# Performance work log

Hardware: AMD Instinct MI355X
Metric: run time of the kernel (lower is better)

Reference implementation:

```python
import jax, jax.numpy as jnp
import numpy as np

H = 128  # hidden_size


def lstm_layer(x, Wih, Whh, bih, bhh):
    """Unidirectional LSTM layer, batch_first input x: [B, T, I] -> [B, T, H].
    PyTorch gate order: i, f, g, o."""
    B = x.shape[0]
    # precompute input projections as one big GEMM: [B, T, 4H]
    xp = jnp.einsum('bti,gi->btg', x, Wih) + bih + bhh
    xp = jnp.transpose(xp, (1, 0, 2))  # [T, B, 4H]
    h0 = jnp.zeros((B, H), x.dtype)
    c0 = jnp.zeros((B, H), x.dtype)

    def step(carry, xp_t):
        h, c = carry
        gates = xp_t + h @ Whh.T  # [B, 4H]
        i, f, g, o = jnp.split(gates, 4, axis=-1)
        i = jax.nn.sigmoid(i)
        f = jax.nn.sigmoid(f)
        g = jnp.tanh(g)
        o = jax.nn.sigmoid(o)
        c = f * c + i * g
        h = o * jnp.tanh(c)
        return (h, c), h

    (_, _), ys = jax.lax.scan(step, (h0, c0), xp)
    return jnp.transpose(ys, (1, 0, 2))  # [B, T, H]


def setup_inputs() -> dict:
    key = jax.random.key(0)
    ks = jax.random.split(key, 13)
    s = 0.05
    inp = {
        'x': jax.random.normal(ks[0], (8, 1, 102400), jnp.float32),
        'Wih0': jax.random.normal(ks[1], (4 * H, 1), jnp.float32) * s,
        'Whh0': jax.random.normal(ks[2], (4 * H, H), jnp.float32) * s,
        'bih0': jnp.zeros((4 * H,), jnp.float32),
        'bhh0': jnp.zeros((4 * H,), jnp.float32).at[H:2 * H].set(1.0),
        'Wih1': jax.random.normal(ks[3], (4 * H, H), jnp.float32) * s,
        'Whh1': jax.random.normal(ks[4], (4 * H, H), jnp.float32) * s,
        'bih1': jnp.zeros((4 * H,), jnp.float32),
        'bhh1': jnp.zeros((4 * H,), jnp.float32).at[H:2 * H].set(1.0),
        'fcW1': jax.random.normal(ks[5], (H // 2, H), jnp.float32) * s,
        'fcb1': jnp.zeros((H // 2,), jnp.float32),
        'fcW2': jax.random.normal(ks[6], (11, H // 2), jnp.float32) * s,
        'fcb2': jnp.zeros((11,), jnp.float32),
    }
    return inp


def reference(x, Wih0, Whh0, bih0, bhh0, Wih1, Whh1, bih1, bhh1,
              fcW1, fcb1, fcW2, fcb2):
    # x: [B, 1, L] -> [B, L, 1]  (transpose(1, 2))
    x = jnp.transpose(x, (0, 2, 1))
    h1 = lstm_layer(x, Wih0, Whh0, bih0, bhh0)   # [B, T, H]
    h2 = lstm_layer(h1, Wih1, Whh1, bih1, bhh1)  # [B, T, H]
    pooled = jnp.mean(h2, axis=1)                # [B, H]; dropout is identity in eval
    hid = jax.nn.relu(pooled @ fcW1.T + fcb1)    # [B, H//2]
    logits = hid @ fcW2.T + fcb2                 # [B, 11]
    return logits
```

## Files before the change

kernel.cpp:

```cpp
#include <hip/hip_runtime.h>

#define HH 128
#define G4 512
#define TT 102400
#define BB 8

typedef _Float16 v2h __attribute__((ext_vector_type(2)));

#if __has_builtin(__builtin_amdgcn_fdot2)
#define FDOT2(a, b, c) __builtin_amdgcn_fdot2((a), (b), (c), false)
#else
static __device__ __forceinline__ float fdot2_fb(v2h a, v2h b, float c) {
    return fmaf((float)a[0], (float)b[0], fmaf((float)a[1], (float)b[1], c));
}
#define FDOT2(a, b, c) fdot2_fb((a), (b), (c))
#endif

template<int CTRL>
__device__ __forceinline__ float dpp_mov(float v) {
    return __int_as_float(
        __builtin_amdgcn_update_dpp(0, __float_as_int(v), CTRL, 0xF, 0xF, true));
}

__device__ __forceinline__ float tanh_f(float x) {
    return fmaf(2.0f, __builtin_amdgcn_rcpf(1.0f + __expf(-2.0f * x)), -1.0f);
}

union HI { int i; v2h h; };

__device__ __forceinline__ float dotred(const v2h w[8][8],
                                        const _Float16* __restrict__ hsl,
                                        bool bp1, bool bp2, bool bp3) {
    const int4* hp4 = (const int4*)hsl;
    int4 ha = hp4[0], hb = hp4[1];
    int hp[8] = {ha.x, ha.y, ha.z, ha.w, hb.x, hb.y, hb.z, hb.w};
    float acc[8];
#pragma unroll
    for (int r = 0; r < 8; ++r) acc[r] = 0.f;
#pragma unroll
    for (int i = 0; i < 8; ++i) {
        HI u; u.i = hp[i];
#pragma unroll
        for (int r = 0; r < 8; ++r) acc[r] = FDOT2(w[r][i], u.h, acc[r]);
    }
    float b0[4];
#pragma unroll
    for (int m = 0; m < 4; ++m) {
        float send = bp1 ? acc[2 * m] : acc[2 * m + 1];
        float keep = bp1 ? acc[2 * m + 1] : acc[2 * m];
        b0[m] = keep + dpp_mov<0xB1>(send);
    }
    float d0[2];
#pragma unroll
    for (int i = 0; i < 2; ++i) {
        float send = bp2 ? b0[i] : b0[i + 2];
        float keep = bp2 ? b0[i + 2] : b0[i];
        d0[i] = keep + dpp_mov<0x4E>(send);
    }
    float send = bp3 ? d0[0] : d0[1];
    float keep = bp3 ? d0[1] : d0[0];
    return keep + dpp_mov<0x141>(send);
}

__device__ __forceinline__ void load_w8h(const float* __restrict__ W,
                                         int Q, int j, v2h w[8][8]) {
#pragma unroll
    for (int r = 0; r < 8; ++r) {
        int row = 2 * Q + (r & 1) + 128 * (r >> 1);
        const float4* rp = (const float4*)(W + (size_t)row * HH + 16 * j);
#pragma unroll
        for (int i = 0; i < 4; ++i) {
            float4 f = rp[i];
            w[r][2 * i]     = (v2h){(_Float16)f.x, (_Float16)f.y};
            w[r][2 * i + 1] = (v2h){(_Float16)f.z, (_Float16)f.w};
        }
    }
}

__global__ void __launch_bounds__(512, 2)
lstm_slot_kernel(
    const float* __restrict__ x,
    const float* __restrict__ Wih0, const float* __restrict__ Whh0,
    const float* __restrict__ bih0, const float* __restrict__ bhh0,
    const float* __restrict__ Wih1, const float* __restrict__ Whh1,
    const float* __restrict__ bih1, const float* __restrict__ bhh1,
    float* __restrict__ h1s, float* __restrict__ c1s,
    float* __restrict__ h2s, float* __restrict__ c2s,
    double* __restrict__ pooled,
    _Float16* __restrict__ h1ring,
    float* __restrict__ xpring,
    int c, int chunkT, int nchunks)
{
    __shared__ __align__(32) _Float16 hh[2 * HH];
    const int t = threadIdx.x;
    const int Q = t >> 3;
    const int j = t & 7;
    const bool bp1 = ((j ^ (j >> 2)) & 1) != 0;
    const bool bp2 = ((j ^ (j >> 1)) & 1) != 0;
    const bool bp3 = ((j >> 2) & 1) != 0;
    const int cellj = bp1 ? 1 : 0;
    const int gatej = (bp2 ? 2 : 0) + (bp3 ? 1 : 0);
    const int myc   = 2 * Q + cellj;
    const int myrow = myc + 128 * gatej;
    const bool owner = (gatej == 0);
    const bool isg = (gatej == 2);
    const float fe = isg ? -2.f : -1.f;
    const float fm = isg ?  2.f :  1.f;
    const float fa = isg ? -1.f :  0.f;

    if (blockIdx.x < 16) {
        const bool isA = (blockIdx.x < 8);
        const int cc = isA ? c : (c - 2);
        if (cc < 0 || cc >= nchunks) return;
        const int b = blockIdx.x & 7;

        v2h w[8][8];
        load_w8h(isA ? Whh0 : Whh1, Q, j, w);
        float bias_l = 0.f, wih_l = 0.f;
        if (isA) { bias_l = bih0[myrow] + bhh0[myrow]; wih_l = Wih0[myrow]; }

        float* hst = isA ? h1s : h2s;
        float* cst = isA ? c1s : c2s;
        float c_reg = cst[b * HH + myc];
        if (t < HH) hh[t] = (_Float16)hst[b * HH + t];

        _Float16* ringp = h1ring + ((size_t)((c & 1) * BB + b)) * (size_t)chunkT * HH;
        const float4* xb4 = (const float4*)(x + (size_t)b * TT + (size_t)cc * chunkT);
        const float* xps = xpring
            + ((size_t)((cc & 1) * BB + b)) * (size_t)chunkT * G4 + 4 * myc + gatej;

        const int nt4 = chunkT >> 2;
        float4 xq = {0, 0, 0, 0};
        float xpc[4] = {0, 0, 0, 0};
        if (isA) xq = xb4[0];
        else {
#pragma unroll
            for (int u = 0; u < 4; ++u) xpc[u] = xps[(size_t)u * G4];
        }
        double pacc = 0.0;
        float hfin = 0.f;
        __syncthreads();

        for (int t4 = 0; t4 < nt4; ++t4) {
            float4 xqn = {0, 0, 0, 0};
            float xpn[4] = {0, 0, 0, 0};
            if (isA) {
                if (t4 + 1 < nt4) xqn = xb4[t4 + 1];
            } else if (t4 + 1 < nt4) {
#pragma unroll
                for (int u = 0; u < 4; ++u)
                    xpn[u] = xps[(size_t)(t4 * 4 + 4 + u) * G4];
            }
#pragma unroll
            for (int u = 0; u < 4; ++u) {
                const int buf = u & 1;
                float sfin = dotred(w, hh + buf * HH + 16 * j, bp1, bp2, bp3);
                float pre;
                if (isA) {
                    float xt = (u == 0) ? xq.x : (u == 1) ? xq.y
                             : (u == 2) ? xq.z : xq.w;
                    pre = fmaf(xt, wih_l, sfin + bias_l);
                } else {
                    pre = sfin + xpc[u];
                }
                float e  = __expf(pre * fe);
                float rr = __builtin_amdgcn_rcpf(1.0f + e);
                float act = fmaf(fm, rr, fa);
                float t1 = dpp_mov<0x141>(act);
                float t2 = dpp_mov<0x4E>(act);
                float t3 = dpp_mov<0x4E>(t1);
                c_reg = fmaf(t1, c_reg, act * t2);
                float th = tanh_f(c_reg);
                float hv = t3 * th;
                hfin = hv;
                if (owner) {
                    hh[(buf ^ 1) * HH + myc] = (_Float16)hv;
                    if (isA) ringp[(size_t)(t4 * 4 + u) * HH + myc] = (_Float16)hv;
                    else     pacc += (double)hv;
                }
                __syncthreads();
            }
            xq = xqn;
            if (!isA) {
#pragma unroll
                for (int u = 0; u < 4; ++u) xpc[u] = xpn[u];
            }
        }
        if (owner) {
            cst[b * HH + myc] = c_reg;
            hst[b * HH + myc] = hfin;
            if (!isA) pooled[b * HH + myc] += pacc;
        }

    } else {
        const int bc = c - 1;
        if (bc < 0 || bc >= nchunks) return;
        const int ib = blockIdx.x - 16;
        const int bb = ib >> 3;
        const int sl = ib & 7;
        v2h w[8][8];
        load_w8h(Wih1, Q, j, w);
        const float bias_l = bih1[myrow] + bhh1[myrow];
        const _Float16* hrp = h1ring
            + ((size_t)((bc & 1) * BB + bb)) * (size_t)chunkT * HH;
        float* xpw = xpring + ((size_t)((bc & 1) * BB + bb)) * (size_t)chunkT * G4;
        if (t < HH) hh[t] = hrp[(size_t)sl * HH + t];
        __syncthreads();
        int pb = 0;
        for (int tt = sl; tt < chunkT; tt += 8) {
            int ttn = tt + 8;
            bool pf = (t < HH) && (ttn < chunkT);
            _Float16 hn = (_Float16)0.f;
            if (pf) hn = hrp[(size_t)ttn * HH + t];
            float sfin = dotred(w, hh + pb * HH + 16 * j, bp1, bp2, bp3);
            if (pf) hh[(pb ^ 1) * HH + t] = hn;
            xpw[(size_t)tt * G4 + 4 * myc + gatej] = sfin + bias_l;
            __syncthreads();
            pb ^= 1;
        }
    }
}

__global__ void head_kernel(const double* __restrict__ pooled,
                            const float* __restrict__ fcW1, const float* __restrict__ fcb1,
                            const float* __restrict__ fcW2, const float* __restrict__ fcb2,
                            float* __restrict__ out)
{
    __shared__ float p_s[HH];
    __shared__ float hid_s[64];
    const int b = blockIdx.x, t = threadIdx.x;
    if (t < HH) p_s[t] = (float)(pooled[b * HH + t] * (1.0 / (double)TT));
    __syncthreads();
    if (t < 64) {
        float acc = fcb1[t];
#pragma unroll 8
        for (int k = 0; k < HH; ++k) acc = fmaf(p_s[k], fcW1[t * HH + k], acc);
        hid_s[t] = fmaxf(acc, 0.f);
    }
    __syncthreads();
    if (t < 11) {
        float acc = fcb2[t];
#pragma unroll
        for (int k = 0; k < 64; ++k) acc = fmaf(hid_s[k], fcW2[t * 64 + k], acc);
        out[b * 11 + t] = acc;
    }
}

extern "C" void kernel_launch(void* const* d_in, const int* in_sizes, int n_in,
                              void* d_out, int out_size, void* d_ws, size_t ws_size,
                              hipStream_t stream)
{
    const float* x    = (const float*)d_in[0];
    const float* Wih0 = (const float*)d_in[1];
    const float* Whh0 = (const float*)d_in[2];
    const float* bih0 = (const float*)d_in[3];
    const float* bhh0 = (const float*)d_in[4];
    const float* Wih1 = (const float*)d_in[5];
    const float* Whh1 = (const float*)d_in[6];
    const float* bih1 = (const float*)d_in[7];
    const float* bhh1 = (const float*)d_in[8];
    const float* fcW1 = (const float*)d_in[9];
    const float* fcb1 = (const float*)d_in[10];
    const float* fcW2 = (const float*)d_in[11];
    const float* fcb2 = (const float*)d_in[12];
    float* out = (float*)d_out;

    char* wsp = (char*)d_ws;
    float*  h1s    = (float*) (wsp + 0);
    float*  c1s    = (float*) (wsp + 4096);
    float*  h2s    = (float*) (wsp + 8192);
    float*  c2s    = (float*) (wsp + 12288);
    double* pooled = (double*)(wsp + 16384);
    const size_t STATE_BYTES = 24576;

    static const int cands[] = {3200, 1600, 800, 400, 160, 80, 40, 8};
    int chunkT = 8;
    for (int i = 0; i < 8; ++i) {
        size_t need = STATE_BYTES + (size_t)36864 * (size_t)cands[i];
        if (need <= ws_size) { chunkT = cands[i]; break; }
    }
    const int nchunks = TT / chunkT;

    _Float16* h1ring = (_Float16*)(wsp + STATE_BYTES);
    float* xpring = (float*)(wsp + STATE_BYTES + (size_t)2 * BB * chunkT * HH * 2);

    hipMemsetAsync(d_ws, 0, STATE_BYTES, stream);

    const int nslots = nchunks + 2;
    for (int c = 0; c < nslots; ++c) {
        lstm_slot_kernel<<<80, 512, 0, stream>>>(
            x, Wih0, Whh0, bih0, bhh0, Wih1, Whh1, bih1, bhh1,
            h1s, c1s, h2s, c2s, pooled, h1ring, xpring,
            c, chunkT, nchunks);
    }
    head_kernel<<<BB, 128, 0, stream>>>(pooled, fcW1, fcb1, fcW2, fcb2, out);
}
```

Baseline: 62.78 ms.

## Batch all recurrences into one block per layer using MFMA 16x16x32

The recurrent matvec for each LSTM layer moves from one block per batch element using fdot2 plus DPP gate exchange to a single block per layer. That block computes all 8 batch columns with MFMA f16 16x16x32 instructions. The batch sits in the N dimension, duplicated into both halves so each lane can finish two cells with every gate locally, without cross-lane shuffles. The intent is to shorten the per-timestep serial latency and drop the 16 recurrent blocks to 2. The cost is a dependent MFMA chain per step and wider per-step xp loads, and the grid shrinks to 66 blocks.

```diff
diff --git a/kernel.cpp b/kernel.cpp
--- a/kernel.cpp
+++ b/kernel.cpp
@@ -4,8 +4,14 @@
 #define G4 512
 #define TT 102400
 #define BB 8
+#define HS 144
+#define HBUFH (BB * HS)
 
 typedef _Float16 v2h __attribute__((ext_vector_type(2)));
+typedef _Float16 v8h __attribute__((ext_vector_type(8)));
+typedef float f32x4 __attribute__((ext_vector_type(4)));
+
+#define MFMA16(a, b, c) __builtin_amdgcn_mfma_f32_16x16x32_f16((a), (b), (c), 0, 0, 0)
 
 #if __has_builtin(__builtin_amdgcn_fdot2)
 #define FDOT2(a, b, c) __builtin_amdgcn_fdot2((a), (b), (c), false)
@@ -22,6 +28,9 @@
         __builtin_amdgcn_update_dpp(0, __float_as_int(v), CTRL, 0xF, 0xF, true));
 }
 
+__device__ __forceinline__ float sig_f(float x) {
+    return __builtin_amdgcn_rcpf(1.0f + __expf(-x));
+}
 __device__ __forceinline__ float tanh_f(float x) {
     return fmaf(2.0f, __builtin_amdgcn_rcpf(1.0f + __expf(-2.0f * x)), -1.0f);
 }
@@ -91,120 +100,176 @@
     float* __restrict__ xpring,
     int c, int chunkT, int nchunks)
 {
-    __shared__ __align__(32) _Float16 hh[2 * HH];
+    __shared__ __align__(16) _Float16 hsh[2 * HBUFH];
     const int t = threadIdx.x;
-    const int Q = t >> 3;
-    const int j = t & 7;
-    const bool bp1 = ((j ^ (j >> 2)) & 1) != 0;
-    const bool bp2 = ((j ^ (j >> 1)) & 1) != 0;
-    const bool bp3 = ((j >> 2) & 1) != 0;
-    const int cellj = bp1 ? 1 : 0;
-    const int gatej = (bp2 ? 2 : 0) + (bp3 ? 1 : 0);
-    const int myc   = 2 * Q + cellj;
-    const int myrow = myc + 128 * gatej;
-    const bool owner = (gatej == 0);
-    const bool isg = (gatej == 2);
-    const float fe = isg ? -2.f : -1.f;
-    const float fm = isg ?  2.f :  1.f;
-    const float fa = isg ? -1.f :  0.f;
-
-    if (blockIdx.x < 16) {
-        const bool isA = (blockIdx.x < 8);
+
+    if (blockIdx.x < 2) {
+        const bool isA = (blockIdx.x == 0);
         const int cc = isA ? c : (c - 2);
         if (cc < 0 || cc >= nchunks) return;
-        const int b = blockIdx.x & 7;
-
-        v2h w[8][8];
-        load_w8h(isA ? Whh0 : Whh1, Q, j, w);
-        float bias_l = 0.f, wih_l = 0.f;
-        if (isA) { bias_l = bih0[myrow] + bhh0[myrow]; wih_l = Wih0[myrow]; }
-
+        const int lane = t & 63, wv = t >> 6;
+        const int quad = lane >> 4, n16 = lane & 15, nb = lane & 7;
+        const int hi = (lane >> 3) & 1;
+        const int mrow0 = 16 * wv;
+        const int myc0 = mrow0 + quad * 4 + 2 * hi;
+
+        v8h a[4][4];
+        const float* Wl = isA ? Whh0 : Whh1;
+#pragma unroll
+        for (int g = 0; g < 4; ++g)
+#pragma unroll
+            for (int kt = 0; kt < 4; ++kt) {
+                const float* rp = Wl + (size_t)(mrow0 + n16 + 128 * g) * HH
+                                + 32 * kt + quad * 8;
+                v8h av;
+#pragma unroll
+                for (int e = 0; e < 8; ++e) av[e] = (_Float16)rp[e];
+                a[g][kt] = av;
+            }
+        f32x4 biasf[4];
+#pragma unroll
+        for (int g = 0; g < 4; ++g) {
+            f32x4 bv = {0.f, 0.f, 0.f, 0.f};
+            if (isA) {
+#pragma unroll
+                for (int r = 0; r < 4; ++r) {
+                    int row = mrow0 + quad * 4 + r + 128 * g;
+                    bv[r] = bih0[row] + bhh0[row];
+                }
+            }
+            biasf[g] = bv;
+        }
+        float wih2[4][2];
+        if (isA) {
+#pragma unroll
+            for (int g = 0; g < 4; ++g)
+#pragma unroll
+                for (int e = 0; e < 2; ++e)
+                    wih2[g][e] = Wih0[myc0 + e + 128 * g];
+        }
+        float* cst = isA ? c1s : c2s;
         float* hst = isA ? h1s : h2s;
-        float* cst = isA ? c1s : c2s;
-        float c_reg = cst[b * HH + myc];
-        if (t < HH) hh[t] = (_Float16)hst[b * HH + t];
-
-        _Float16* ringp = h1ring + ((size_t)((c & 1) * BB + b)) * (size_t)chunkT * HH;
-        const float4* xb4 = (const float4*)(x + (size_t)b * TT + (size_t)cc * chunkT);
+        float cr0 = cst[nb * HH + myc0], cr1 = cst[nb * HH + myc0 + 1];
+        hsh[nb * HS + myc0]     = (_Float16)hst[nb * HH + myc0];
+        hsh[nb * HS + myc0 + 1] = (_Float16)hst[nb * HH + myc0 + 1];
+
+        _Float16* ringp = h1ring + ((size_t)((c & 1) * BB + nb)) * (size_t)chunkT * HH;
         const float* xps = xpring
-            + ((size_t)((cc & 1) * BB + b)) * (size_t)chunkT * G4 + 4 * myc + gatej;
-
+            + ((size_t)((cc & 1) * BB + nb)) * (size_t)chunkT * G4 + 4 * myc0;
+        const float4* xb4 = (const float4*)(x + (size_t)nb * TT + (size_t)cc * chunkT);
         const int nt4 = chunkT >> 2;
-        float4 xq = {0, 0, 0, 0};
-        float xpc[4] = {0, 0, 0, 0};
-        if (isA) xq = xb4[0];
-        else {
-#pragma unroll
-            for (int u = 0; u < 4; ++u) xpc[u] = xps[(size_t)u * G4];
-        }
-        double pacc = 0.0;
-        float hfin = 0.f;
+
+        float4 xcur = {0, 0, 0, 0}, xnxt = {0, 0, 0, 0};
+        float4 xpc[4][2], xpn[4][2];
+        if (isA) {
+            xcur = xb4[0];
+        } else {
+#pragma unroll
+            for (int u = 0; u < 4; ++u) {
+                const float4* p = (const float4*)(xps + (size_t)u * G4);
+                xpc[u][0] = p[0]; xpc[u][1] = p[1];
+            }
+        }
+        float h0 = 0.f, h1 = 0.f;
+        double pa0 = 0.0, pa1 = 0.0;
         __syncthreads();
 
         for (int t4 = 0; t4 < nt4; ++t4) {
-            float4 xqn = {0, 0, 0, 0};
-            float xpn[4] = {0, 0, 0, 0};
-            if (isA) {
-                if (t4 + 1 < nt4) xqn = xb4[t4 + 1];
-            } else if (t4 + 1 < nt4) {
-#pragma unroll
-                for (int u = 0; u < 4; ++u)
-                    xpn[u] = xps[(size_t)(t4 * 4 + 4 + u) * G4];
-            }
+            if (isA) xnxt = (t4 + 1 < nt4) ? xb4[t4 + 1] : xcur;
 #pragma unroll
             for (int u = 0; u < 4; ++u) {
                 const int buf = u & 1;
-                float sfin = dotred(w, hh + buf * HH + 16 * j, bp1, bp2, bp3);
-                float pre;
+                if (!isA) {
+                    int pg = (t4 + 1 < nt4) ? (t4 + 1) : t4;
+                    const float4* p = (const float4*)(xps + (size_t)(pg * 4 + u) * G4);
+                    xpn[u][0] = p[0]; xpn[u][1] = p[1];
+                }
+                const _Float16* hb = hsh + buf * HBUFH + nb * HS + 8 * quad;
+                v8h bf0 = *(const v8h*)(hb);
+                v8h bf1 = *(const v8h*)(hb + 32);
+                v8h bf2 = *(const v8h*)(hb + 64);
+                v8h bf3 = *(const v8h*)(hb + 96);
+                f32x4 d0 = biasf[0], d1 = biasf[1], d2 = biasf[2], d3 = biasf[3];
+                d0 = MFMA16(a[0][0], bf0, d0); d1 = MFMA16(a[1][0], bf0, d1);
+                d2 = MFMA16(a[2][0], bf0, d2); d3 = MFMA16(a[3][0], bf0, d3);
+                d0 = MFMA16(a[0][1], bf1, d0); d1 = MFMA16(a[1][1], bf1, d1);
+                d2 = MFMA16(a[2][1], bf1, d2); d3 = MFMA16(a[3][1], bf1, d3);
+                d0 = MFMA16(a[0][2], bf2, d0); d1 = MFMA16(a[1][2], bf2, d1);
+                d2 = MFMA16(a[2][2], bf2, d2); d3 = MFMA16(a[3][2], bf2, d3);
+                d0 = MFMA16(a[0][3], bf3, d0); d1 = MFMA16(a[1][3], bf3, d1);
+                d2 = MFMA16(a[2][3], bf3, d2); d3 = MFMA16(a[3][3], bf3, d3);
+                float p00 = hi ? d0[2] : d0[0], p01 = hi ? d0[3] : d0[1];
+                float p10 = hi ? d1[2] : d1[0], p11 = hi ? d1[3] : d1[1];
+                float p20 = hi ? d2[2] : d2[0], p21 = hi ? d2[3] : d2[1];
+                float p30 = hi ? d3[2] : d3[0], p31 = hi ? d3[3] : d3[1];
                 if (isA) {
-                    float xt = (u == 0) ? xq.x : (u == 1) ? xq.y
-                             : (u == 2) ? xq.z : xq.w;
-                    pre = fmaf(xt, wih_l, sfin + bias_l);
+                    float xt = (u == 0) ? xcur.x : (u == 1) ? xcur.y
+                             : (u == 2) ? xcur.z : xcur.w;
+                    p00 = fmaf(xt, wih2[0][0], p00); p01 = fmaf(xt, wih2[0][1], p01);
+                    p10 = fmaf(xt, wih2[1][0], p10); p11 = fmaf(xt, wih2[1][1], p11);
+                    p20 = fmaf(xt, wih2[2][0], p20); p21 = fmaf(xt, wih2[2][1], p21);
+                    p30 = fmaf(xt, wih2[3][0], p30); p31 = fmaf(xt, wih2[3][1], p31);
                 } else {
-                    pre = sfin + xpc[u];
-                }
-                float e  = __expf(pre * fe);
-                float rr = __builtin_amdgcn_rcpf(1.0f + e);
-                float act = fmaf(fm, rr, fa);
-                float t1 = dpp_mov<0x141>(act);
-                float t2 = dpp_mov<0x4E>(act);
-                float t3 = dpp_mov<0x4E>(t1);
-                c_reg = fmaf(t1, c_reg, act * t2);
-                float th = tanh_f(c_reg);
-                float hv = t3 * th;
-                hfin = hv;
-                if (owner) {
-                    hh[(buf ^ 1) * HH + myc] = (_Float16)hv;
-                    if (isA) ringp[(size_t)(t4 * 4 + u) * HH + myc] = (_Float16)hv;
-                    else     pacc += (double)hv;
+                    p00 += xpc[u][0].x; p10 += xpc[u][0].y;
+                    p20 += xpc[u][0].z; p30 += xpc[u][0].w;
+                    p01 += xpc[u][1].x; p11 += xpc[u][1].y;
+                    p21 += xpc[u][1].z; p31 += xpc[u][1].w;
+                }
+                float i0 = sig_f(p00), f0 = sig_f(p10);
+                float g0 = tanh_f(p20), o0 = sig_f(p30);
+                float i1 = sig_f(p01), f1 = sig_f(p11);
+                float g1 = tanh_f(p21), o1 = sig_f(p31);
+                cr0 = fmaf(f0, cr0, i0 * g0);
+                cr1 = fmaf(f1, cr1, i1 * g1);
+                h0 = o0 * tanh_f(cr0);
+                h1 = o1 * tanh_f(cr1);
+                v2h hp; hp[0] = (_Float16)h0; hp[1] = (_Float16)h1;
+                *(v2h*)(hsh + (buf ^ 1) * HBUFH + nb * HS + myc0) = hp;
+                if (isA) {
+                    *(v2h*)(ringp + (size_t)(t4 * 4 + u) * HH + myc0) = hp;
+                } else {
+                    pa0 += (double)h0; pa1 += (double)h1;
                 }
                 __syncthreads();
             }
-            xq = xqn;
+            xcur = xnxt;
             if (!isA) {
 #pragma unroll
-                for (int u = 0; u < 4; ++u) xpc[u] = xpn[u];
-            }
-        }
-        if (owner) {
-            cst[b * HH + myc] = c_reg;
-            hst[b * HH + myc] = hfin;
-            if (!isA) pooled[b * HH + myc] += pacc;
+                for (int u = 0; u < 4; ++u) {
+                    xpc[u][0] = xpn[u][0]; xpc[u][1] = xpn[u][1];
+                }
+            }
+        }
+        cst[nb * HH + myc0]     = cr0;
+        cst[nb * HH + myc0 + 1] = cr1;
+        hst[nb * HH + myc0]     = h0;
+        hst[nb * HH + myc0 + 1] = h1;
+        if (!isA) {
+            pooled[nb * HH + myc0]     += pa0;
+            pooled[nb * HH + myc0 + 1] += pa1;
         }
 
     } else {
         const int bc = c - 1;
         if (bc < 0 || bc >= nchunks) return;
-        const int ib = blockIdx.x - 16;
+        const int ib = blockIdx.x - 2;
         const int bb = ib >> 3;
         const int sl = ib & 7;
+        const int Q = t >> 3, j = t & 7;
+        const bool bp1 = ((j ^ (j >> 2)) & 1) != 0;
+        const bool bp2 = ((j ^ (j >> 1)) & 1) != 0;
+        const bool bp3 = ((j >> 2) & 1) != 0;
+        const int cellj = bp1 ? 1 : 0;
+        const int gatej = (bp2 ? 2 : 0) + (bp3 ? 1 : 0);
+        const int myc = 2 * Q + cellj;
+        const int myrow = myc + 128 * gatej;
         v2h w[8][8];
         load_w8h(Wih1, Q, j, w);
         const float bias_l = bih1[myrow] + bhh1[myrow];
         const _Float16* hrp = h1ring
             + ((size_t)((bc & 1) * BB + bb)) * (size_t)chunkT * HH;
         float* xpw = xpring + ((size_t)((bc & 1) * BB + bb)) * (size_t)chunkT * G4;
-        if (t < HH) hh[t] = hrp[(size_t)sl * HH + t];
+        if (t < HH) hsh[t] = hrp[(size_t)sl * HH + t];
         __syncthreads();
         int pb = 0;
         for (int tt = sl; tt < chunkT; tt += 8) {
@@ -212,8 +277,8 @@
             bool pf = (t < HH) && (ttn < chunkT);
             _Float16 hn = (_Float16)0.f;
             if (pf) hn = hrp[(size_t)ttn * HH + t];
-            float sfin = dotred(w, hh + pb * HH + 16 * j, bp1, bp2, bp3);
-            if (pf) hh[(pb ^ 1) * HH + t] = hn;
+            float sfin = dotred(w, hsh + pb * HH + 16 * j, bp1, bp2, bp3);
+            if (pf) hsh[(pb ^ 1) * HH + t] = hn;
             xpw[(size_t)tt * G4 + 4 * myc + gatej] = sfin + bias_l;
             __syncthreads();
             pb ^= 1;
@@ -288,7 +353,7 @@
 
     const int nslots = nchunks + 2;
     for (int c = 0; c < nslots; ++c) {
-        lstm_slot_kernel<<<80, 512, 0, stream>>>(
+        lstm_slot_kernel<<<66, 512, 0, stream>>>(
             x, Wih0, Whh0, bih0, bhh0, Wih1, Whh1, bih1, bhh1,
             h1s, c1s, h2s, c2s, pooled, h1ring, xpring,
             c, chunkT, nchunks);
```

Result: slower. 79.58 ms (+26.8%).

## Process two batch rows per recurrent block to halve recurrence blocks

Applied to the files above, without the earlier changes.

Each recurrent-layer block now advances two batch sequences (b and b+4) in lockstep, sharing the register-resident Whh weights and a single barrier per timestep. The grid shrinks from 80 to 72 blocks, with 4 blocks per LSTM layer instead of 8. The aim is to interleave two independent dependency chains so each block hides latency better and needs fewer barriers per unit of work. The cost is a longer per-step critical path, since each step now does two dot reductions, and higher register pressure from the duplicated state.

```diff
diff --git a/kernel.cpp b/kernel.cpp
--- a/kernel.cpp
+++ b/kernel.cpp
@@ -91,7 +91,7 @@
     float* __restrict__ xpring,
     int c, int chunkT, int nchunks)
 {
-    __shared__ __align__(32) _Float16 hh[2 * HH];
+    __shared__ __align__(32) _Float16 hh[512];
     const int t = threadIdx.x;
     const int Q = t >> 3;
     const int j = t & 7;
@@ -108,11 +108,12 @@
     const float fm = isg ?  2.f :  1.f;
     const float fa = isg ? -1.f :  0.f;
 
-    if (blockIdx.x < 16) {
-        const bool isA = (blockIdx.x < 8);
+    if (blockIdx.x < 8) {
+        const bool isA = (blockIdx.x < 4);
         const int cc = isA ? c : (c - 2);
         if (cc < 0 || cc >= nchunks) return;
-        const int b = blockIdx.x & 7;
+        const int b0 = blockIdx.x & 3;
+        const int b1 = b0 + 4;
 
         v2h w[8][8];
         load_w8h(isA ? Whh0 : Whh1, Q, j, w);
@@ -121,81 +122,120 @@
 
         float* hst = isA ? h1s : h2s;
         float* cst = isA ? c1s : c2s;
-        float c_reg = cst[b * HH + myc];
-        if (t < HH) hh[t] = (_Float16)hst[b * HH + t];
-
-        _Float16* ringp = h1ring + ((size_t)((c & 1) * BB + b)) * (size_t)chunkT * HH;
-        const float4* xb4 = (const float4*)(x + (size_t)b * TT + (size_t)cc * chunkT);
-        const float* xps = xpring
-            + ((size_t)((cc & 1) * BB + b)) * (size_t)chunkT * G4 + 4 * myc + gatej;
+        float cr0 = cst[b0 * HH + myc];
+        float cr1 = cst[b1 * HH + myc];
+        if (t < HH) {
+            hh[t]       = (_Float16)hst[b0 * HH + t];
+            hh[HH + t]  = (_Float16)hst[b1 * HH + t];
+        }
+
+        _Float16* ring0 = h1ring + ((size_t)((c & 1) * BB + b0)) * (size_t)chunkT * HH;
+        _Float16* ring1 = h1ring + ((size_t)((c & 1) * BB + b1)) * (size_t)chunkT * HH;
+        const float4* xb0 = (const float4*)(x + (size_t)b0 * TT + (size_t)cc * chunkT);
+        const float4* xb1 = (const float4*)(x + (size_t)b1 * TT + (size_t)cc * chunkT);
+        const float* xps0 = xpring
+            + ((size_t)((cc & 1) * BB + b0)) * (size_t)chunkT * G4 + 4 * myc + gatej;
+        const float* xps1 = xpring
+            + ((size_t)((cc & 1) * BB + b1)) * (size_t)chunkT * G4 + 4 * myc + gatej;
 
         const int nt4 = chunkT >> 2;
-        float4 xq = {0, 0, 0, 0};
-        float xpc[4] = {0, 0, 0, 0};
-        if (isA) xq = xb4[0];
-        else {
-#pragma unroll
-            for (int u = 0; u < 4; ++u) xpc[u] = xps[(size_t)u * G4];
-        }
-        double pacc = 0.0;
-        float hfin = 0.f;
+        float4 xq0 = {0, 0, 0, 0}, xq1 = {0, 0, 0, 0};
+        float xpc0[4] = {0, 0, 0, 0}, xpc1[4] = {0, 0, 0, 0};
+        if (isA) {
+            xq0 = xb0[0]; xq1 = xb1[0];
+        } else {
+#pragma unroll
+            for (int u = 0; u < 4; ++u) {
+                xpc0[u] = xps0[(size_t)u * G4];
+                xpc1[u] = xps1[(size_t)u * G4];
+            }
+        }
+        double pa0 = 0.0, pa1 = 0.0;
+        float hf0 = 0.f, hf1 = 0.f;
         __syncthreads();
 
         for (int t4 = 0; t4 < nt4; ++t4) {
-            float4 xqn = {0, 0, 0, 0};
-            float xpn[4] = {0, 0, 0, 0};
+            float4 xn0 = {0, 0, 0, 0}, xn1 = {0, 0, 0, 0};
+            float xpn0[4] = {0, 0, 0, 0}, xpn1[4] = {0, 0, 0, 0};
             if (isA) {
-                if (t4 + 1 < nt4) xqn = xb4[t4 + 1];
+                if (t4 + 1 < nt4) { xn0 = xb0[t4 + 1]; xn1 = xb1[t4 + 1]; }
             } else if (t4 + 1 < nt4) {
 #pragma unroll
-                for (int u = 0; u < 4; ++u)
-                    xpn[u] = xps[(size_t)(t4 * 4 + 4 + u) * G4];
+                for (int u = 0; u < 4; ++u) {
+                    xpn0[u] = xps0[(size_t)(t4 * 4 + 4 + u) * G4];
+                    xpn1[u] = xps1[(size_t)(t4 * 4 + 4 + u) * G4];
+                }
             }
 #pragma unroll
             for (int u = 0; u < 4; ++u) {
                 const int buf = u & 1;
-                float sfin = dotred(w, hh + buf * HH + 16 * j, bp1, bp2, bp3);
-                float pre;
+                float s0 = dotred(w, hh + buf * 256 + 16 * j,       bp1, bp2, bp3);
+                float s1 = dotred(w, hh + buf * 256 + HH + 16 * j,  bp1, bp2, bp3);
+                float pre0, pre1;
                 if (isA) {
-                    float xt = (u == 0) ? xq.x : (u == 1) ? xq.y
-                             : (u == 2) ? xq.z : xq.w;
-                    pre = fmaf(xt, wih_l, sfin + bias_l);
+                    float xt0 = (u == 0) ? xq0.x : (u == 1) ? xq0.y
+                              : (u == 2) ? xq0.z : xq0.w;
+                    float xt1 = (u == 0) ? xq1.x : (u == 1) ? xq1.y
+                              : (u == 2) ? xq1.z : xq1.w;
+                    pre0 = fmaf(xt0, wih_l, s0 + bias_l);
+                    pre1 = fmaf(xt1, wih_l, s1 + bias_l);
                 } else {
-                    pre = sfin + xpc[u];
+                    pre0 = s0 + xpc0[u];
+                    pre1 = s1 + xpc1[u];
                 }
-                float e  = __expf(pre * fe);
-                float rr = __builtin_amdgcn_rcpf(1.0f + e);
-                float act = fmaf(fm, rr, fa);
-                float t1 = dpp_mov<0x141>(act);
-                float t2 = dpp_mov<0x4E>(act);
-                float t3 = dpp_mov<0x4E>(t1);
-                c_reg = fmaf(t1, c_reg, act * t2);
-                float th = tanh_f(c_reg);
-                float hv = t3 * th;
-                hfin = hv;
+                float e0  = __expf(pre0 * fe);
+                float e1  = __expf(pre1 * fe);
+                float r0 = __builtin_amdgcn_rcpf(1.0f + e0);
+                float r1 = __builtin_amdgcn_rcpf(1.0f + e1);
+                float a0 = fmaf(fm, r0, fa);
+                float a1 = fmaf(fm, r1, fa);
+                float f0 = dpp_mov<0x141>(a0);
+                float f1 = dpp_mov<0x141>(a1);
+                float g0 = dpp_mov<0x4E>(a0);
+                float g1 = dpp_mov<0x4E>(a1);
+                float o0 = dpp_mov<0x4E>(f0);
+                float o1 = dpp_mov<0x4E>(f1);
+                cr0 = fmaf(f0, cr0, a0 * g0);
+                cr1 = fmaf(f1, cr1, a1 * g1);
+                float th0 = tanh_f(cr0);
+                float th1 = tanh_f(cr1);
+                float hv0 = o0 * th0;
+                float hv1 = o1 * th1;
+                hf0 = hv0; hf1 = hv1;
                 if (owner) {
-                    hh[(buf ^ 1) * HH + myc] = (_Float16)hv;
-                    if (isA) ringp[(size_t)(t4 * 4 + u) * HH + myc] = (_Float16)hv;
-                    else     pacc += (double)hv;
+                    hh[(buf ^ 1) * 256 + myc]      = (_Float16)hv0;
+                    hh[(buf ^ 1) * 256 + HH + myc] = (_Float16)hv1;
+                    if (isA) {
+                        ring0[(size_t)(t4 * 4 + u) * HH + myc] = (_Float16)hv0;
+                        ring1[(size_t)(t4 * 4 + u) * HH + myc] = (_Float16)hv1;
+                    } else {
+                        pa0 += (double)hv0;
+                        pa1 += (double)hv1;
+                    }
                 }
                 __syncthreads();
             }
-            xq = xqn;
+            xq0 = xn0; xq1 = xn1;
             if (!isA) {
 #pragma unroll
-                for (int u = 0; u < 4; ++u) xpc[u] = xpn[u];
+                for (int u = 0; u < 4; ++u) { xpc0[u] = xpn0[u]; xpc1[u] = xpn1[u]; }
             }
         }
         if (owner) {
-            cst[b * HH + myc] = c_reg;
-            hst[b * HH + myc] = hfin;
-            if (!isA) pooled[b * HH + myc] += pacc;
+            cst[b0 * HH + myc] = cr0;
+            cst[b1 * HH + myc] = cr1;
+            hst[b0 * HH + myc] = hf0;
+            hst[b1 * HH + myc] = hf1;
+            if (!isA) {
+                pooled[b0 * HH + myc] += pa0;
+                pooled[b1 * HH + myc] += pa1;
+            }
         }
 
     } else {
         const int bc = c - 1;
         if (bc < 0 || bc >= nchunks) return;
-        const int ib = blockIdx.x - 16;
+        const int ib = blockIdx.x - 8;
         const int bb = ib >> 3;
         const int sl = ib & 7;
         v2h w[8][8];
@@ -288,7 +328,7 @@
 
     const int nslots = nchunks + 2;
     for (int c = 0; c < nslots; ++c) {
-        lstm_slot_kernel<<<80, 512, 0, stream>>>(
+        lstm_slot_kernel<<<72, 512, 0, stream>>>(
             x, Wih0, Whh0, bih0, bhh0, Wih1, Whh1, bih1, bhh1,
             h1s, c1s, h2s, c2s, pooled, h1ring, xpring,
             c, chunkT, nchunks);
```

After: 115.3 ms. 1.84x slower.
